# Optimization experiments

Measured on AMD Instinct MI355X. Metric: run time of the kernel, lower is better.

The kernel has to match this reference:

```python
import jax, jax.numpy as jnp
import numpy as np

N_NODES = 100000
N_EDGES = 3200000
C = 50           # out_channels (== in_channels here, so no zero-padding needed)
L = 3            # num_layers
EDGE_TYPES = 2


def setup_inputs() -> dict:
    key = jax.random.key(0)
    ks = jax.random.split(key, 12)
    s = 1.0 / np.sqrt(C)
    x = jax.random.normal(ks[0], (N_NODES, C), dtype=jnp.float32)
    edge_index = jax.random.randint(ks[1], (2, N_EDGES), 0, N_NODES)
    edge_attr = jax.random.randint(ks[2], (N_EDGES,), 0, EDGE_TYPES)
    conv_weight = jax.random.uniform(ks[3], (L, C, C), jnp.float32, -s, s)
    w_ih = jax.random.uniform(ks[4], (3 * C, C), jnp.float32, -s, s)
    w_hh = jax.random.uniform(ks[5], (3 * C, C), jnp.float32, -s, s)
    b_ih = jax.random.uniform(ks[6], (3 * C,), jnp.float32, -s, s)
    b_hh = jax.random.uniform(ks[7], (3 * C,), jnp.float32, -s, s)
    edge_emb = jax.random.normal(ks[8], (EDGE_TYPES, C), dtype=jnp.float32)
    lin_w = jax.random.uniform(ks[9], (C, C), jnp.float32, -s, s)
    lin_b = jax.random.uniform(ks[10], (C,), jnp.float32, -s, s)
    return dict(x=x, edge_index=edge_index, edge_attr=edge_attr,
                conv_weight=conv_weight, w_ih=w_ih, w_hh=w_hh,
                b_ih=b_ih, b_hh=b_hh, edge_emb=edge_emb,
                lin_w=lin_w, lin_b=lin_b)


def _gru_cell(m, h, w_ih, w_hh, b_ih, b_hh):
    # torch.nn.GRUCell math
    gi = m @ w_ih.T + b_ih            # [N, 3C]
    gh = h @ w_hh.T + b_hh            # [N, 3C]
    i_r, i_z, i_n = jnp.split(gi, 3, axis=-1)
    h_r, h_z, h_n = jnp.split(gh, 3, axis=-1)
    r = jax.nn.sigmoid(i_r + h_r)
    z = jax.nn.sigmoid(i_z + h_z)
    n = jnp.tanh(i_n + r * h_n)
    return (1.0 - z) * n + z * h


def reference(x, edge_index, edge_attr, conv_weight, w_ih, w_hh,
              b_ih, b_hh, edge_emb, lin_w, lin_b):
    # edge embeddings are computed but unused in the original forward
    _ = edge_emb[edge_attr]
    src, dst = edge_index[0], edge_index[1]  # flow: source -> target
    h = x  # in_channels == out_channels, so no padding
    for i in range(L):
        m = h @ conv_weight[i]                               # [N, C]
        msg = jnp.take(m, src, axis=0)                       # gather  [E, C]
        agg = jax.ops.segment_sum(msg, dst, num_segments=N_NODES)  # scatter-add
        h = _gru_cell(agg, h, w_ih, w_hh, b_ih, b_hh)
    out = jax.nn.relu(h) @ lin_w.T + lin_b
    return out
```

## Files before the change

kernel.cpp:

```cpp
#include <hip/hip_runtime.h>
#include <hip/hip_fp16.h>

#define N_NODES 100000
#define N_EDGES 3200000
#define C 50
#define PH 64
#define NH (N_NODES * PH)
#define NTILES (N_NODES / 16)
#define NB2 391
#define BSH2 8
#define BMSK2 255
#define BCAP2 9216
#define EPB 4096
#define EB  ((N_EDGES + EPB - 1) / EPB)
#define EPT (EPB / 256)

typedef _Float16 half8 __attribute__((ext_vector_type(8)));
typedef float floatx4 __attribute__((ext_vector_type(4)));


__global__ __launch_bounds__(256) void partition_kernel(const int* __restrict__ ei,
                                                        int* __restrict__ cnt,
                                                        unsigned int* __restrict__ pairs) {
    __shared__ int hist[NB2];
    __shared__ int base[NB2];
    int e0 = blockIdx.x * EPB;
    int b[EPT]; unsigned int p[EPT];
#pragma unroll
    for (int i = 0; i < EPT; ++i) {
        int e = e0 + i * 256 + threadIdx.x;
        bool ok = e < N_EDGES;
        int d = ok ? ei[N_EDGES + e] : 0;
        int s = ok ? ei[e] : 0;
        b[i] = ok ? (d >> BSH2) : -1;
        p[i] = ((unsigned)s << BSH2) | (unsigned)(d & BMSK2);
    }
    for (int t = threadIdx.x; t < NB2; t += 256) hist[t] = 0;
    __syncthreads();
#pragma unroll
    for (int i = 0; i < EPT; ++i)
        if (b[i] >= 0) atomicAdd(&hist[b[i]], 1);
    __syncthreads();
    for (int t = threadIdx.x; t < NB2; t += 256)
        base[t] = hist[t] ? (t * BCAP2 + atomicAdd(&cnt[t], hist[t])) : 0;
    __syncthreads();
    for (int t = threadIdx.x; t < NB2; t += 256) hist[t] = 0;
    __syncthreads();
#pragma unroll
    for (int i = 0; i < EPT; ++i) {
        if (b[i] >= 0) {
            int r = atomicAdd(&hist[b[i]], 1);
            pairs[base[b[i]] + r] = p[i];
        }
    }
}

__global__ __launch_bounds__(1024) void bscan_kernel(const int* __restrict__ cnt,
                                                     int* __restrict__ bucketOff) {
    __shared__ int buf[1024];
    int t = threadIdx.x;
    int v = (t < NB2) ? cnt[t] : 0;
    buf[t] = v;
    __syncthreads();
    for (int off = 1; off < 1024; off <<= 1) {
        int tv = (t >= off) ? buf[t - off] : 0;
        __syncthreads();
        buf[t] += tv;
        __syncthreads();
    }
    if (t < NB2) {
        int excl = buf[t] - v;
        bucketOff[t] = excl;
        if (t == NB2 - 1) bucketOff[NB2] = excl + v;
    }
}

__global__ __launch_bounds__(256) void bucket_fill_kernel(const unsigned int* __restrict__ pairs,
                                                          const int* __restrict__ cnt,
                                                          const int* __restrict__ bucketOff,
                                                          int* __restrict__ rowptr,
                                                          int* __restrict__ col) {
    __shared__ int deg[256];
    __shared__ int cur[256];
    int b = blockIdx.x;
    int nbase = b << BSH2;
    int n_e = cnt[b];
    int slot0 = b * BCAP2;
    int segB = bucketOff[b];
    int tid = threadIdx.x;
    deg[tid] = 0;
    __syncthreads();
    for (int e = tid; e < n_e; e += 256)
        atomicAdd(&deg[pairs[slot0 + e] & BMSK2], 1);
    __syncthreads();
    int v = deg[tid];
    cur[tid] = v;
    __syncthreads();
    for (int off = 1; off < 256; off <<= 1) {
        int t = (tid >= off) ? cur[tid - off] : 0;
        __syncthreads();
        cur[tid] += t;
        __syncthreads();
    }
    int excl = cur[tid] - v;
    int n = nbase + tid;
    if (n < N_NODES) rowptr[n] = segB + excl;
    __syncthreads();
    cur[tid] = excl;
    __syncthreads();
    for (int e = tid; e < n_e; e += 256) {
        unsigned int p = pairs[slot0 + e];
        int r = atomicAdd(&cur[p & BMSK2], 1);
        col[segB + r] = (int)(p >> BSH2);
    }
    if (b == 0 && tid == 0) rowptr[N_NODES] = N_EDGES;
}

__global__ __launch_bounds__(256) void init_kernel(const float* __restrict__ x,
                                                   const float* __restrict__ conv_w,
                                                   const float* __restrict__ w_ih,
                                                   const float* __restrict__ w_hh,
                                                   const float* __restrict__ lin_w,
                                                   _Float16* __restrict__ h0,
                                                   _Float16* __restrict__ wb,
                                                   int* __restrict__ cnt) {
    int t = blockIdx.x * 256 + threadIdx.x;
    if (t < NH) {
        int n = t >> 6, c = t & 63;
        h0[t] = (c < C) ? (_Float16)x[n * C + c] : (_Float16)0.f;
    }
    if (t < 13 * 4096) {
        int mat = t >> 12, idx = t & 4095, n = idx >> 6, k = idx & 63;
        float v = 0.f;
        if (n < C && k < C) {
            if (mat < 9) {
                int l = mat / 3, g = mat - l * 3;
                const float* wl = conv_w + l * C * C + k * C;
                const float* wi = w_ih + (g * C + n) * C;
                float acc = 0.f;
#pragma unroll
                for (int j = 0; j < C; ++j) acc = fmaf(wl[j], wi[j], acc);
                v = acc;
            } else if (mat < 12) {
                v = w_hh[((mat - 9) * C + n) * C + k];
            } else {
                v = lin_w[n * C + k];
            }
        }
        wb[t] = (_Float16)v;
    }
    if (t < NB2) cnt[t] = 0;
}

__device__ inline half8 load_a16(const _Float16* __restrict__ base, int row, int ks, int lane) {
    return *(const half8*)(base + (size_t)row * PH + (ks << 5) + ((lane >> 4) << 3));
}

__device__ inline half8 load_b_frag(const _Float16* __restrict__ wb, int nt, int ks, int lane) {
    const _Float16* p = wb + (((nt << 4) + (lane & 15)) << 6) + (ks << 5) + ((lane >> 4) << 3);
    return *(const half8*)p;
}

__device__ inline half8 load_b_lds(const _Float16* swb, int mat, int nt, int ks, int lane) {
    return *(const half8*)(swb + mat * 4608 + ((nt << 4) + (lane & 15)) * 72 + (ks << 5) + ((lane >> 4) << 3));
}

__device__ inline float sigmoidf_(float x) { return 1.f / (1.f + __expf(-x)); }
__device__ inline float tanhf_(float x)    { return 2.f * sigmoidf_(2.f * x) - 1.f; }

__device__ inline void stage_swb(_Float16* swb, const _Float16* ihp, const _Float16* hhp) {
    for (int i = threadIdx.x; i < 3072; i += 256) {
        int g = i << 3;
        int m = g >> 12, rem = g & 4095, row = rem >> 6, colc = rem & 63;
        const _Float16* src = (m < 3) ? (ihp + g) : (hhp + (g - 3 * 4096));
        *(half8*)&swb[m * 4608 + row * 72 + colc] = *(const half8*)src;
    }
}

__global__ __launch_bounds__(256) void gemm_gru(const _Float16* __restrict__ agg,
                                                const _Float16* __restrict__ hin,
                                                const _Float16* __restrict__ wb_ihc,
                                                const _Float16* __restrict__ wb_hh,
                                                const float* __restrict__ b_ih,
                                                const float* __restrict__ b_hh,
                                                _Float16* __restrict__ hout) {
    __shared__ __align__(16) _Float16 swb[6 * 4608];
    __shared__ __align__(16) _Float16 hlds[4][16][72];
    int wid = threadIdx.x >> 6, lane = threadIdx.x & 63;
    int tile = blockIdx.x * 4 + wid;
    bool act = tile < NTILES;
    int base = tile * 16;
    int lrow = lane & 15, lgrp = lane >> 4;
    stage_swb(swb, wb_ihc, wb_hh);
    half8 aA[2], aH[2];
    if (act) {
        int arow = base + lrow;
#pragma unroll
        for (int ks = 0; ks < 2; ++ks) {
            aA[ks] = load_a16(agg, arow, ks, lane);
            aH[ks] = load_a16(hin, arow, ks, lane);
        }
        *(half8*)&hlds[wid][lrow][lgrp << 3]        = aH[0];
        *(half8*)&hlds[wid][lrow][32 + (lgrp << 3)] = aH[1];
    }
    __syncthreads();
    if (!act) return;
#pragma unroll
    for (int nt = 0; nt < 4; ++nt) {
        int colc = (nt << 4) + lrow;
        bool cok = colc < C;
        float r_[4], z_[4];
        {
            floatx4 aI = {0.f,0.f,0.f,0.f}, aHc = {0.f,0.f,0.f,0.f};
#pragma unroll
            for (int ks = 0; ks < 2; ++ks) {
                aI  = __builtin_amdgcn_mfma_f32_16x16x32_f16(aA[ks], load_b_lds(swb, 0, nt, ks, lane), aI, 0, 0, 0);
                aHc = __builtin_amdgcn_mfma_f32_16x16x32_f16(aH[ks], load_b_lds(swb, 3, nt, ks, lane), aHc, 0, 0, 0);
            }
            float bi = cok ? b_ih[colc] : 0.f;
            float bh = cok ? b_hh[colc] : 0.f;
#pragma unroll
            for (int e = 0; e < 4; ++e) r_[e] = sigmoidf_((aI[e] + bi) + (aHc[e] + bh));
        }
        {
            floatx4 aI = {0.f,0.f,0.f,0.f}, aHc = {0.f,0.f,0.f,0.f};
#pragma unroll
            for (int ks = 0; ks < 2; ++ks) {
                aI  = __builtin_amdgcn_mfma_f32_16x16x32_f16(aA[ks], load_b_lds(swb, 1, nt, ks, lane), aI, 0, 0, 0);
                aHc = __builtin_amdgcn_mfma_f32_16x16x32_f16(aH[ks], load_b_lds(swb, 4, nt, ks, lane), aHc, 0, 0, 0);
            }
            float bi = cok ? b_ih[C + colc] : 0.f;
            float bh = cok ? b_hh[C + colc] : 0.f;
#pragma unroll
            for (int e = 0; e < 4; ++e) z_[e] = sigmoidf_((aI[e] + bi) + (aHc[e] + bh));
        }
        {
            floatx4 aI = {0.f,0.f,0.f,0.f}, aHc = {0.f,0.f,0.f,0.f};
#pragma unroll
            for (int ks = 0; ks < 2; ++ks) {
                aI  = __builtin_amdgcn_mfma_f32_16x16x32_f16(aA[ks], load_b_lds(swb, 2, nt, ks, lane), aI, 0, 0, 0);
                aHc = __builtin_amdgcn_mfma_f32_16x16x32_f16(aH[ks], load_b_lds(swb, 5, nt, ks, lane), aHc, 0, 0, 0);
            }
            float bi = cok ? b_ih[2 * C + colc] : 0.f;
            float bh = cok ? b_hh[2 * C + colc] : 0.f;
#pragma unroll
            for (int e = 0; e < 4; ++e) {
                int rl = (lgrp << 2) + e;
                int row = base + rl;
                _Float16 val = (_Float16)0.f;
                if (cok) {
                    float hv = (float)hlds[wid][rl][colc];
                    float nn = tanhf_((aI[e] + bi) + r_[e] * (aHc[e] + bh));
                    float z = z_[e];
                    val = (_Float16)((1.f - z) * nn + z * hv);
                }
                hout[(size_t)row * PH + colc] = val;
            }
        }
    }
}

__global__ __launch_bounds__(256) void gemm_gru_out(const _Float16* __restrict__ agg,
                                                    const _Float16* __restrict__ hin,
                                                    const _Float16* __restrict__ wb_ihc,
                                                    const _Float16* __restrict__ wb_hh,
                                                    const float* __restrict__ b_ih,
                                                    const float* __restrict__ b_hh,
                                                    const _Float16* __restrict__ wb_out,
                                                    const float* __restrict__ lin_b,
                                                    float* __restrict__ out) {
    __shared__ __align__(16) _Float16 swb[6 * 4608];
    __shared__ __align__(16) _Float16 hlds[4][16][72];
    int wid = threadIdx.x >> 6, lane = threadIdx.x & 63;
    int tile = blockIdx.x * 4 + wid;
    bool act = tile < NTILES;
    int base = tile * 16;
    int lrow = lane & 15, lgrp = lane >> 4;
    stage_swb(swb, wb_ihc, wb_hh);
    half8 aA[2], aH[2];
    if (act) {
        int arow = base + lrow;
#pragma unroll
        for (int ks = 0; ks < 2; ++ks) {
            aA[ks] = load_a16(agg, arow, ks, lane);
            aH[ks] = load_a16(hin, arow, ks, lane);
        }
        *(half8*)&hlds[wid][lrow][lgrp << 3]        = aH[0];
        *(half8*)&hlds[wid][lrow][32 + (lgrp << 3)] = aH[1];
    }
    __syncthreads();
    if (act) {
#pragma unroll
        for (int nt = 0; nt < 4; ++nt) {
            int colc = (nt << 4) + lrow;
            bool cok = colc < C;
            float r_[4], z_[4];
            {
                floatx4 aI = {0.f,0.f,0.f,0.f}, aHc = {0.f,0.f,0.f,0.f};
#pragma unroll
                for (int ks = 0; ks < 2; ++ks) {
                    aI  = __builtin_amdgcn_mfma_f32_16x16x32_f16(aA[ks], load_b_lds(swb, 0, nt, ks, lane), aI, 0, 0, 0);
                    aHc = __builtin_amdgcn_mfma_f32_16x16x32_f16(aH[ks], load_b_lds(swb, 3, nt, ks, lane), aHc, 0, 0, 0);
                }
                float bi = cok ? b_ih[colc] : 0.f;
                float bh = cok ? b_hh[colc] : 0.f;
#pragma unroll
                for (int e = 0; e < 4; ++e) r_[e] = sigmoidf_((aI[e] + bi) + (aHc[e] + bh));
            }
            {
                floatx4 aI = {0.f,0.f,0.f,0.f}, aHc = {0.f,0.f,0.f,0.f};
#pragma unroll
                for (int ks = 0; ks < 2; ++ks) {
                    aI  = __builtin_amdgcn_mfma_f32_16x16x32_f16(aA[ks], load_b_lds(swb, 1, nt, ks, lane), aI, 0, 0, 0);
                    aHc = __builtin_amdgcn_mfma_f32_16x16x32_f16(aH[ks], load_b_lds(swb, 4, nt, ks, lane), aHc, 0, 0, 0);
                }
                float bi = cok ? b_ih[C + colc] : 0.f;
                float bh = cok ? b_hh[C + colc] : 0.f;
#pragma unroll
                for (int e = 0; e < 4; ++e) z_[e] = sigmoidf_((aI[e] + bi) + (aHc[e] + bh));
            }
            {
                floatx4 aI = {0.f,0.f,0.f,0.f}, aHc = {0.f,0.f,0.f,0.f};
#pragma unroll
                for (int ks = 0; ks < 2; ++ks) {
                    aI  = __builtin_amdgcn_mfma_f32_16x16x32_f16(aA[ks], load_b_lds(swb, 2, nt, ks, lane), aI, 0, 0, 0);
                    aHc = __builtin_amdgcn_mfma_f32_16x16x32_f16(aH[ks], load_b_lds(swb, 5, nt, ks, lane), aHc, 0, 0, 0);
                }
                float bi = cok ? b_ih[2 * C + colc] : 0.f;
                float bh = cok ? b_hh[2 * C + colc] : 0.f;
#pragma unroll
                for (int e = 0; e < 4; ++e) {
                    int rl = (lgrp << 2) + e;
                    _Float16 val = (_Float16)0.f;
                    if (cok) {
                        float hv = (float)hlds[wid][rl][colc];
                        float nn = tanhf_((aI[e] + bi) + r_[e] * (aHc[e] + bh));
                        float z = z_[e];
                        float h3 = (1.f - z) * nn + z * hv;
                        val = (_Float16)(h3 > 0.f ? h3 : 0.f);
                    }
                    hlds[wid][rl][colc] = val;
                }
            }
        }
    }
    __syncthreads();
    if (act) {
        half8 a0 = *(const half8*)&hlds[wid][lrow][lgrp << 3];
        half8 a1 = *(const half8*)&hlds[wid][lrow][32 + (lgrp << 3)];
#pragma unroll
        for (int nt = 0; nt < 4; ++nt) {
            floatx4 acc = {0.f, 0.f, 0.f, 0.f};
            acc = __builtin_amdgcn_mfma_f32_16x16x32_f16(a0, load_b_frag(wb_out, nt, 0, lane), acc, 0, 0, 0);
            acc = __builtin_amdgcn_mfma_f32_16x16x32_f16(a1, load_b_frag(wb_out, nt, 1, lane), acc, 0, 0, 0);
            int col = (nt << 4) + lrow;
            if (col < C) {
                float b = lin_b[col];
#pragma unroll
                for (int e = 0; e < 4; ++e) {
                    int row = base + (lgrp << 2) + e;
                    out[(size_t)row * C + col] = acc[e] + b;
                }
            }
        }
    }
}

__global__ __launch_bounds__(256) void gather_kernel(const __half* __restrict__ h,
                                                     const int* __restrict__ rowptr,
                                                     const int* __restrict__ col,
                                                     _Float16* __restrict__ agg) {
    int w = (blockIdx.x * 256 + threadIdx.x) >> 6;
    int lane = threadIdx.x & 63;
    if (w >= N_NODES) return;
    int start = rowptr[w], end = rowptr[w + 1];
    int j = lane >> 3, q = lane & 7;
    bool qok = (q < 7);
    int hoff = qok ? (q * 8) : 48;
    float acc0 = 0.f, acc1 = 0.f, acc2 = 0.f, acc3 = 0.f;
    float acc4 = 0.f, acc5 = 0.f, acc6 = 0.f, acc7 = 0.f;

    for (int base = start; base < end; base += 64) {
        int cidx = base + lane;
        int cols = col[cidx < N_EDGES ? cidx : (N_EDGES - 1)];
        int cnt = end - base; if (cnt > 64) cnt = 64;
        int nt8 = (cnt + 7) >> 3;
#pragma unroll 4
        for (int t = 0; t < nt8; ++t) {
            int rel = 8 * t + j;
            int s = __shfl(cols, rel);
            bool valid = qok && (rel < cnt);
            const uint4 v = *reinterpret_cast<const uint4*>(h + (size_t)s * PH + hoff);
            float2 f0 = __half22float2(*reinterpret_cast<const __half2*>(&v.x));
            float2 f1 = __half22float2(*reinterpret_cast<const __half2*>(&v.y));
            float2 f2 = __half22float2(*reinterpret_cast<const __half2*>(&v.z));
            float2 f3 = __half22float2(*reinterpret_cast<const __half2*>(&v.w));
            acc0 += valid ? f0.x : 0.f;  acc1 += valid ? f0.y : 0.f;
            acc2 += valid ? f1.x : 0.f;  acc3 += valid ? f1.y : 0.f;
            acc4 += valid ? f2.x : 0.f;  acc5 += valid ? f2.y : 0.f;
            acc6 += valid ? f3.x : 0.f;  acc7 += valid ? f3.y : 0.f;
        }
    }
#pragma unroll
    for (int s = 8; s <= 32; s <<= 1) {
        acc0 += __shfl_xor(acc0, s); acc1 += __shfl_xor(acc1, s);
        acc2 += __shfl_xor(acc2, s); acc3 += __shfl_xor(acc3, s);
        acc4 += __shfl_xor(acc4, s); acc5 += __shfl_xor(acc5, s);
        acc6 += __shfl_xor(acc6, s); acc7 += __shfl_xor(acc7, s);
    }
    if (j == 0) {
        if (qok) {
            half8 o;
            o[0] = (_Float16)acc0; o[1] = (_Float16)acc1;
            o[2] = (_Float16)acc2; o[3] = (_Float16)acc3;
            o[4] = (_Float16)acc4; o[5] = (_Float16)acc5;
            o[6] = (_Float16)acc6; o[7] = (_Float16)acc7;
            *reinterpret_cast<half8*>(agg + (size_t)w * PH + q * 8) = o;
        } else {
            half8 z = {};
            *reinterpret_cast<half8*>(agg + (size_t)w * PH + 56) = z;
        }
    }
}

extern "C" void kernel_launch(void* const* d_in, const int* in_sizes, int n_in,
                              void* d_out, int out_size, void* d_ws, size_t ws_size,
                              hipStream_t stream) {
    const float* x      = (const float*)d_in[0];
    const int*   ei     = (const int*)  d_in[1];
    const float* conv_w = (const float*)d_in[3];
    const float* w_ih   = (const float*)d_in[4];
    const float* w_hh   = (const float*)d_in[5];
    const float* b_ih   = (const float*)d_in[6];
    const float* b_hh   = (const float*)d_in[7];
    const float* lin_w  = (const float*)d_in[9];
    const float* lin_b  = (const float*)d_in[10];
    float* out = (float*)d_out;

    _Float16* h0  = (_Float16*)d_ws;
    _Float16* h1  = h0 + NH;
    _Float16* agg = h1 + NH;
    _Float16* scratch = agg + NH;
    _Float16* wb  = scratch + NH;
    unsigned int* pairs = (unsigned int*)agg;
    int* col       = (int*)(wb + 13 * 4096);
    int* rowptr    = col + N_EDGES;
    int* cnt       = rowptr + N_NODES + 1;
    int* bucketOff = cnt + NB2;

    const int initBlocks = (NH + 255) / 256;
    const int waveBlocks = (N_NODES * 64 + 255) / 256;
    const int gemmBlocks = (NTILES + 3) / 4;

    init_kernel<<<initBlocks, 256, 0, stream>>>(x, conv_w, w_ih, w_hh, lin_w, h0, wb, cnt);

    partition_kernel<<<EB, 256, 0, stream>>>(ei, cnt, pairs);
    bscan_kernel<<<1, 1024, 0, stream>>>(cnt, bucketOff);
    bucket_fill_kernel<<<NB2, 256, 0, stream>>>(pairs, cnt, bucketOff, rowptr, col);

    gather_kernel<<<waveBlocks, 256, 0, stream>>>((const __half*)h0, rowptr, col, agg);
    gemm_gru<<<gemmBlocks, 256, 0, stream>>>(agg, h0, wb + 0 * 3 * 4096, wb + 9 * 4096,
                                             b_ih, b_hh, h1);
    gather_kernel<<<waveBlocks, 256, 0, stream>>>((const __half*)h1, rowptr, col, agg);
    gemm_gru<<<gemmBlocks, 256, 0, stream>>>(agg, h1, wb + 1 * 3 * 4096, wb + 9 * 4096,
                                             b_ih, b_hh, h0);
    gather_kernel<<<waveBlocks, 256, 0, stream>>>((const __half*)h0, rowptr, col, agg);
    gemm_gru_out<<<gemmBlocks, 256, 0, stream>>>(agg, h0, wb + 2 * 3 * 4096, wb + 9 * 4096,
                                                 b_ih, b_hh, wb + 12 * 4096, lin_b, out);
}
```

Before: 355.7 us.

## Split gather into four source-range passes for cache locality

The CSR build now sub-sorts each node's incoming edges by source range (four ranges of 25000 nodes) and records four row pointers per node. The gather runs as four passes, each touching only one quarter of the feature table, so that the working set of random reads fits better in cache. The cost is four launches per layer, re-reading and rewriting the agg buffer, and an extra fp16 rounding step at each pass. It also makes the row-pointer array four times larger.

```diff
diff --git a/kernel.cpp b/kernel.cpp
--- a/kernel.cpp
+++ b/kernel.cpp
@@ -14,6 +14,8 @@
 #define EPB 4096
 #define EB  ((N_EDGES + EPB - 1) / EPB)
 #define EPT (EPB / 256)
+#define NSR 4
+#define SRDIV 25000
 
 typedef _Float16 half8 __attribute__((ext_vector_type(8)));
 typedef float floatx4 __attribute__((ext_vector_type(4)));
@@ -78,42 +80,53 @@
 __global__ __launch_bounds__(256) void bucket_fill_kernel(const unsigned int* __restrict__ pairs,
                                                           const int* __restrict__ cnt,
                                                           const int* __restrict__ bucketOff,
-                                                          int* __restrict__ rowptr,
+                                                          int* __restrict__ rowptr2,
                                                           int* __restrict__ col) {
-    __shared__ int deg[256];
-    __shared__ int cur[256];
+    __shared__ int deg[256 * NSR];
+    __shared__ int cur[256 * NSR];
+    __shared__ int tsum[256];
     int b = blockIdx.x;
     int nbase = b << BSH2;
     int n_e = cnt[b];
     int slot0 = b * BCAP2;
     int segB = bucketOff[b];
     int tid = threadIdx.x;
-    deg[tid] = 0;
-    __syncthreads();
-    for (int e = tid; e < n_e; e += 256)
-        atomicAdd(&deg[pairs[slot0 + e] & BMSK2], 1);
-    __syncthreads();
-    int v = deg[tid];
-    cur[tid] = v;
-    __syncthreads();
-    for (int off = 1; off < 256; off <<= 1) {
-        int t = (tid >= off) ? cur[tid - off] : 0;
-        __syncthreads();
-        cur[tid] += t;
-        __syncthreads();
-    }
-    int excl = cur[tid] - v;
-    int n = nbase + tid;
-    if (n < N_NODES) rowptr[n] = segB + excl;
-    __syncthreads();
-    cur[tid] = excl;
+    for (int i = tid; i < 256 * NSR; i += 256) deg[i] = 0;
     __syncthreads();
     for (int e = tid; e < n_e; e += 256) {
         unsigned int p = pairs[slot0 + e];
-        int r = atomicAdd(&cur[p & BMSK2], 1);
+        int idx = ((p & BMSK2) << 2) | ((int)(p >> BSH2) / SRDIV);
+        atomicAdd(&deg[idx], 1);
+    }
+    __syncthreads();
+    int s0 = deg[4 * tid], s1 = deg[4 * tid + 1], s2 = deg[4 * tid + 2], s3 = deg[4 * tid + 3];
+    int tot = s0 + s1 + s2 + s3;
+    tsum[tid] = tot;
+    __syncthreads();
+    for (int off = 1; off < 256; off <<= 1) {
+        int t = (tid >= off) ? tsum[tid - off] : 0;
+        __syncthreads();
+        tsum[tid] += t;
+        __syncthreads();
+    }
+    int c0 = tsum[tid] - tot;
+    int c1 = c0 + s0, c2 = c1 + s1, c3 = c2 + s2;
+    cur[4 * tid] = c0; cur[4 * tid + 1] = c1; cur[4 * tid + 2] = c2; cur[4 * tid + 3] = c3;
+    int n = nbase + tid;
+    if (n < N_NODES) {
+        rowptr2[4 * n]     = segB + c0;
+        rowptr2[4 * n + 1] = segB + c1;
+        rowptr2[4 * n + 2] = segB + c2;
+        rowptr2[4 * n + 3] = segB + c3;
+    }
+    __syncthreads();
+    for (int e = tid; e < n_e; e += 256) {
+        unsigned int p = pairs[slot0 + e];
+        int idx = ((p & BMSK2) << 2) | ((int)(p >> BSH2) / SRDIV);
+        int r = atomicAdd(&cur[idx], 1);
         col[segB + r] = (int)(p >> BSH2);
     }
-    if (b == 0 && tid == 0) rowptr[N_NODES] = N_EDGES;
+    if (b == 0 && tid == 0) rowptr2[4 * N_NODES] = N_EDGES;
 }
 
 __global__ __launch_bounds__(256) void init_kernel(const float* __restrict__ x,
@@ -367,13 +380,14 @@
 }
 
 __global__ __launch_bounds__(256) void gather_kernel(const __half* __restrict__ h,
-                                                     const int* __restrict__ rowptr,
+                                                     const int* __restrict__ rowptr2,
                                                      const int* __restrict__ col,
-                                                     _Float16* __restrict__ agg) {
+                                                     _Float16* __restrict__ agg,
+                                                     int pass) {
     int w = (blockIdx.x * 256 + threadIdx.x) >> 6;
     int lane = threadIdx.x & 63;
     if (w >= N_NODES) return;
-    int start = rowptr[w], end = rowptr[w + 1];
+    int start = rowptr2[w * NSR + pass], end = rowptr2[w * NSR + pass + 1];
     int j = lane >> 3, q = lane & 7;
     bool qok = (q < 7);
     int hoff = qok ? (q * 8) : 48;
@@ -409,16 +423,26 @@
         acc6 += __shfl_xor(acc6, s); acc7 += __shfl_xor(acc7, s);
     }
     if (j == 0) {
-        if (qok) {
-            half8 o;
-            o[0] = (_Float16)acc0; o[1] = (_Float16)acc1;
-            o[2] = (_Float16)acc2; o[3] = (_Float16)acc3;
-            o[4] = (_Float16)acc4; o[5] = (_Float16)acc5;
-            o[6] = (_Float16)acc6; o[7] = (_Float16)acc7;
-            *reinterpret_cast<half8*>(agg + (size_t)w * PH + q * 8) = o;
-        } else {
-            half8 z = {};
-            *reinterpret_cast<half8*>(agg + (size_t)w * PH + 56) = z;
+        _Float16* ar = agg + (size_t)w * PH;
+        if (pass == 0) {
+            if (qok) {
+                half8 o;
+                o[0] = (_Float16)acc0; o[1] = (_Float16)acc1;
+                o[2] = (_Float16)acc2; o[3] = (_Float16)acc3;
+                o[4] = (_Float16)acc4; o[5] = (_Float16)acc5;
+                o[6] = (_Float16)acc6; o[7] = (_Float16)acc7;
+                *reinterpret_cast<half8*>(ar + q * 8) = o;
+            } else {
+                half8 z = {};
+                *reinterpret_cast<half8*>(ar + 56) = z;
+            }
+        } else if (qok && start < end) {
+            half8 o = *reinterpret_cast<half8*>(ar + q * 8);
+            o[0] = (_Float16)((float)o[0] + acc0); o[1] = (_Float16)((float)o[1] + acc1);
+            o[2] = (_Float16)((float)o[2] + acc2); o[3] = (_Float16)((float)o[3] + acc3);
+            o[4] = (_Float16)((float)o[4] + acc4); o[5] = (_Float16)((float)o[5] + acc5);
+            o[6] = (_Float16)((float)o[6] + acc6); o[7] = (_Float16)((float)o[7] + acc7);
+            *reinterpret_cast<half8*>(ar + q * 8) = o;
         }
     }
 }
@@ -444,8 +468,8 @@
     _Float16* wb  = scratch + NH;
     unsigned int* pairs = (unsigned int*)agg;
     int* col       = (int*)(wb + 13 * 4096);
-    int* rowptr    = col + N_EDGES;
-    int* cnt       = rowptr + N_NODES + 1;
+    int* rowptr2   = col + N_EDGES;
+    int* cnt       = rowptr2 + NSR * N_NODES + 1;
     int* bucketOff = cnt + NB2;
 
     const int initBlocks = (NH + 255) / 256;
@@ -456,15 +480,18 @@
 
     partition_kernel<<<EB, 256, 0, stream>>>(ei, cnt, pairs);
     bscan_kernel<<<1, 1024, 0, stream>>>(cnt, bucketOff);
-    bucket_fill_kernel<<<NB2, 256, 0, stream>>>(pairs, cnt, bucketOff, rowptr, col);
-
-    gather_kernel<<<waveBlocks, 256, 0, stream>>>((const __half*)h0, rowptr, col, agg);
+    bucket_fill_kernel<<<NB2, 256, 0, stream>>>(pairs, cnt, bucketOff, rowptr2, col);
+
+    for (int p = 0; p < NSR; ++p)
+        gather_kernel<<<waveBlocks, 256, 0, stream>>>((const __half*)h0, rowptr2, col, agg, p);
     gemm_gru<<<gemmBlocks, 256, 0, stream>>>(agg, h0, wb + 0 * 3 * 4096, wb + 9 * 4096,
                                              b_ih, b_hh, h1);
-    gather_kernel<<<waveBlocks, 256, 0, stream>>>((const __half*)h1, rowptr, col, agg);
+    for (int p = 0; p < NSR; ++p)
+        gather_kernel<<<waveBlocks, 256, 0, stream>>>((const __half*)h1, rowptr2, col, agg, p);
     gemm_gru<<<gemmBlocks, 256, 0, stream>>>(agg, h1, wb + 1 * 3 * 4096, wb + 9 * 4096,
                                              b_ih, b_hh, h0);
-    gather_kernel<<<waveBlocks, 256, 0, stream>>>((const __half*)h0, rowptr, col, agg);
+    for (int p = 0; p < NSR; ++p)
+        gather_kernel<<<waveBlocks, 256, 0, stream>>>((const __half*)h0, rowptr2, col, agg, p);
     gemm_gru_out<<<gemmBlocks, 256, 0, stream>>>(agg, h0, wb + 2 * 3 * 4096, wb + 9 * 4096,
                                                  b_ih, b_hh, wb + 12 * 4096, lin_b, out);
 }
```

After: 611.1 us. +71.8%, slower.
